# Kernel optimization log

Measured on AMD Instinct MI355X. Metric: run time of the kernel, lower is better.

The kernel has to match this reference:

```python
import jax, jax.numpy as jnp
import numpy as np

D_MODEL = 2048
K_DIM = 128
V_DIM = 128
H = 16
B = 1
S = 2048
SCALE_BASE = 512.0
THETA = 10000.0
EPS = 1e-5


def setup_inputs() -> dict:
    key = jax.random.key(0)
    ks = jax.random.split(key, 11)
    lin = lambda k, i, o: jax.random.normal(k, (i, o), jnp.float32) * 0.02
    return {
        "x": jax.random.normal(ks[0], (B, S, D_MODEL), jnp.float32),
        "Wq": lin(ks[1], D_MODEL, K_DIM * H), "bq": jnp.zeros((K_DIM * H,), jnp.float32),
        "Wk": lin(ks[2], D_MODEL, K_DIM * H), "bk": jnp.zeros((K_DIM * H,), jnp.float32),
        "Wv": lin(ks[3], D_MODEL, V_DIM * H), "bv": jnp.zeros((V_DIM * H,), jnp.float32),
        "Wg": lin(ks[4], D_MODEL, V_DIM * H), "bg": jnp.zeros((V_DIM * H,), jnp.float32),
        "Wo": lin(ks[5], V_DIM * H, D_MODEL), "bo": jnp.zeros((D_MODEL,), jnp.float32),
    }


def _rotate_half(x):
    # interleaved pairs: (x0, x1, x2, x3, ...) -> (-x1, x0, -x3, x2, ...)
    xr = x.reshape(*x.shape[:-1], -1, 2)
    x1, x2 = xr[..., 0], xr[..., 1]
    return jnp.stack((-x2, x1), axis=-1).reshape(x.shape)


def _rope_xpos(q, k, seq_len, dim):
    pos = jnp.arange(seq_len, dtype=jnp.float32)
    inv_freq = 1.0 / (THETA ** (jnp.arange(0, dim, 2, dtype=jnp.float32) / dim))
    freqs = jnp.repeat(pos[:, None] * inv_freq[None, :], 2, axis=-1)  # (S, dim)
    cos, sin = jnp.cos(freqs), jnp.sin(freqs)
    sbase = (jnp.arange(0, dim, 2, dtype=jnp.float32) + 0.4 * dim) / (1.4 * dim)
    power = (pos - seq_len // 2) / SCALE_BASE
    scale = jnp.repeat(sbase[None, :] ** power[:, None], 2, axis=-1)  # (S, dim)
    q = (q * cos + _rotate_half(q) * sin) * scale
    k = (k * cos + _rotate_half(k) * sin) / scale
    return q, k


def reference(x, Wq, bq, Wk, bk, Wv, bv, Wg, bg, Wo, bo):
    Bb, Ss, Dd = x.shape
    heads = lambda t: t.reshape(Bb, Ss, H, -1).transpose(0, 2, 1, 3)  # (B,H,S,d)
    q = heads(x @ Wq + bq)
    k = heads(x @ Wk + bk)
    v = heads(x @ Wv + bv)
    q, k = _rope_xpos(q, k, Ss, K_DIM)
    # per-head decay gamma_h = 1 - 2^{-5-h}
    gamma = 1.0 - 2.0 ** (-5.0 - jnp.arange(H, dtype=jnp.float32))
    pos = jnp.arange(Ss, dtype=jnp.float32)
    pm = pos[:, None] - pos[None, :]  # (S,S)
    decay_mask = jnp.where(pm >= 0, gamma[:, None, None] ** jnp.maximum(pm, 0.0), 0.0)  # (H,S,S)
    scores = jnp.einsum('bhid,bhjd->bhij', q, k) * decay_mask
    ret = jnp.einsum('bhij,bhjd->bhid', scores, v)  # (B,H,S,V_DIM)
    # concat heads and GroupNorm (num_groups=H, affine=False) over flattened rows
    concat = ret.transpose(0, 2, 1, 3).reshape(Bb * Ss, H, V_DIM)
    mu = concat.mean(-1, keepdims=True)
    var = ((concat - mu) ** 2).mean(-1, keepdims=True)
    gn = ((concat - mu) / jnp.sqrt(var + EPS)).reshape(Bb, Ss, H * V_DIM)
    out = (jax.nn.silu(x @ Wg + bg) * gn) @ Wo + bo
    return out
```

## Files before the change

### kernel.cpp

```cpp
#include <hip/hip_runtime.h>
#include <hip/hip_bf16.h>

#define S 2048
#define DM 2048
#define H 16
#define HD 128

using bf16 = __hip_bfloat16;
typedef __attribute__((ext_vector_type(8))) short bf16x8;
typedef __attribute__((ext_vector_type(8))) unsigned short u16x8;
typedef __attribute__((ext_vector_type(4))) float f32x4;

__device__ __forceinline__ unsigned short f2bu(float f) {
  bf16 b = __float2bfloat16(f);
  union { bf16 b; unsigned short u; } cv; cv.b = b; return cv.u;
}
__device__ __forceinline__ float bu2f(unsigned short u) {
  union { bf16 b; unsigned short u; } cv; cv.u = u; return __bfloat162float(cv.b);
}

__device__ __forceinline__ void async_copy16(const void* g, void* l) {
  __builtin_amdgcn_global_load_lds(
      (const __attribute__((address_space(1))) void*)g,
      (__attribute__((address_space(3))) void*)l, 16, 0, 0);
}

__global__ __launch_bounds__(256) void cvt_kernel(const float* __restrict__ x,
                                                  unsigned short* __restrict__ o) {
  int i = (blockIdx.x * 256 + threadIdx.x) * 4;
  float4 v = *(const float4*)(x + i);
  ushort4 r;
  r.x = f2bu(v.x); r.y = f2bu(v.y); r.z = f2bu(v.z); r.w = f2bu(v.w);
  *(ushort4*)(o + i) = r;
}

__global__ __launch_bounds__(256) void wtrans_kernel(
    const float* __restrict__ s0, const float* __restrict__ s1, const float* __restrict__ s2,
    const float* __restrict__ s3, const float* __restrict__ s4,
    unsigned short* __restrict__ d0, unsigned short* __restrict__ d1, unsigned short* __restrict__ d2,
    unsigned short* __restrict__ d3, unsigned short* __restrict__ d4) {
  __shared__ float tile[64][65];
  int z = blockIdx.z;
  const float* src = z == 0 ? s0 : z == 1 ? s1 : z == 2 ? s2 : z == 3 ? s3 : s4;
  unsigned short* dst = z == 0 ? d0 : z == 1 ? d1 : z == 2 ? d2 : z == 3 ? d3 : d4;
  int tid = threadIdx.x;
  int by = blockIdx.y * 64;
  int bx = blockIdx.x * 64;
  int r0 = tid >> 4;
  int c0 = (tid & 15) * 4;
#pragma unroll
  for (int i = 0; i < 4; i++) {
    int row = r0 + i * 16;
    float4 t = *(const float4*)(src + (size_t)(by + row) * DM + bx + c0);
    tile[row][c0 + 0] = t.x; tile[row][c0 + 1] = t.y;
    tile[row][c0 + 2] = t.z; tile[row][c0 + 3] = t.w;
  }
  __syncthreads();
#pragma unroll
  for (int i = 0; i < 4; i++) {
    int nrow = r0 + i * 16;
    ushort4 o;
    o.x = f2bu(tile[c0 + 0][nrow]);
    o.y = f2bu(tile[c0 + 1][nrow]);
    o.z = f2bu(tile[c0 + 2][nrow]);
    o.w = f2bu(tile[c0 + 3][nrow]);
    *(ushort4*)(dst + (size_t)(bx + nrow) * DM + by + c0) = o;
  }
}

__device__ __forceinline__ void stage_half(const unsigned short* gbase, char* ldsbase, int tid) {
#pragma unroll
  for (int r = 0; r < 2; r++) {
    int a = r * 8192 + tid * 16;
    int row = a >> 7;
    int cb = (a & 127) ^ ((row & 7) << 4);
    async_copy16((const unsigned char*)(gbase + (size_t)row * DM) + cb, ldsbase + a);
  }
}

__global__ __launch_bounds__(512, 2) void gemm_qkvg_kernel(
    const unsigned short* __restrict__ A, const unsigned short* __restrict__ Bm,
    const float* __restrict__ bias0, const float* __restrict__ bias1,
    const float* __restrict__ bias2, const float* __restrict__ bias3,
    unsigned short* __restrict__ C0, unsigned short* __restrict__ C1,
    unsigned short* __restrict__ Vt, unsigned short* __restrict__ C3) {
  __shared__ alignas(16) char smem[131072];
  char* sA = smem;
  char* sB = smem + 65536;
  int tid = threadIdx.x;
  int wg = blockIdx.y * 32 + blockIdx.x;
  int swz = (wg & 7) * 32 + (wg >> 3);
  int bm = (swz >> 5) * 256;
  int bn = (swz & 31) * 256;
  int wid = tid >> 6, lane = tid & 63;
  int wm = wid >> 2, wn = wid & 3;
  int r16 = lane & 15, quad = lane >> 4;
  f32x4 acc[8][4] = {};
  bf16x8 bfrag[2][4];
  const int bhalf = (wn >> 1) << 14;
  const int blr0 = ((wn & 1) << 6) + r16;

  stage_half(Bm + (size_t)bn * DM, sB, tid);
  stage_half(Bm + (size_t)(bn + 128) * DM, sB + 16384, tid);
  stage_half(A + (size_t)bm * DM, sA, tid);
  stage_half(A + (size_t)(bm + 128) * DM, sA + 16384, tid);
  asm volatile("s_waitcnt vmcnt(0)" ::: "memory");
  __builtin_amdgcn_s_barrier();

  for (int t = 0; t < 32; ++t) {
    const int buf = (t & 1) << 15;
    const int nbuf = buf ^ 32768;
    const bool more = t < 31;
    const int kn = (t + 1) * 64;
    char* sAc = sA + buf;
    char* sBc = sB + buf;
    bf16x8 afrag[4];

#pragma unroll
    for (int nt = 0; nt < 4; ++nt) {
      int lr = blr0 + nt * 16;
      bfrag[0][nt] = *(const bf16x8*)(sBc + bhalf + lr * 128 + ((quad * 16) ^ ((lr & 7) << 4)));
    }
#pragma unroll
    for (int mt = 0; mt < 4; ++mt) {
      int lr = mt * 32 + wm * 16 + r16;
      afrag[mt] = *(const bf16x8*)(sAc + lr * 128 + ((quad * 16) ^ ((lr & 7) << 4)));
    }
    if (more) {
      stage_half(Bm + (size_t)bn * DM + kn, sB + nbuf, tid);
      stage_half(Bm + (size_t)(bn + 128) * DM + kn, sB + nbuf + 16384, tid);
      stage_half(A + (size_t)bm * DM + kn, sA + nbuf, tid);
      stage_half(A + (size_t)(bm + 128) * DM + kn, sA + nbuf + 16384, tid);
    }
    __builtin_amdgcn_s_barrier();
    asm volatile("s_waitcnt lgkmcnt(0)" ::: "memory");
    __builtin_amdgcn_s_setprio(1);
#pragma unroll
    for (int mt = 0; mt < 4; ++mt)
#pragma unroll
      for (int nt = 0; nt < 4; ++nt)
        acc[mt][nt] = __builtin_amdgcn_mfma_f32_16x16x32_bf16(afrag[mt], bfrag[0][nt], acc[mt][nt], 0, 0, 0);
    __builtin_amdgcn_s_setprio(0);

#pragma unroll
    for (int nt = 0; nt < 4; ++nt) {
      int lr = blr0 + nt * 16;
      bfrag[1][nt] = *(const bf16x8*)(sBc + bhalf + lr * 128 + ((64 + quad * 16) ^ ((lr & 7) << 4)));
    }
#pragma unroll
    for (int mt = 0; mt < 4; ++mt) {
      int lr = mt * 32 + wm * 16 + r16;
      afrag[mt] = *(const bf16x8*)(sAc + lr * 128 + ((64 + quad * 16) ^ ((lr & 7) << 4)));
    }
    __builtin_amdgcn_s_barrier();
    asm volatile("s_waitcnt lgkmcnt(0)" ::: "memory");
    __builtin_amdgcn_s_setprio(1);
#pragma unroll
    for (int mt = 0; mt < 4; ++mt)
#pragma unroll
      for (int nt = 0; nt < 4; ++nt)
        acc[mt][nt] = __builtin_amdgcn_mfma_f32_16x16x32_bf16(afrag[mt], bfrag[1][nt], acc[mt][nt], 0, 0, 0);
    __builtin_amdgcn_s_setprio(0);

#pragma unroll
    for (int mt = 0; mt < 4; ++mt) {
      int lr = mt * 32 + wm * 16 + r16;
      afrag[mt] = *(const bf16x8*)(sAc + 16384 + lr * 128 + ((quad * 16) ^ ((lr & 7) << 4)));
    }
    __builtin_amdgcn_s_barrier();
    asm volatile("s_waitcnt lgkmcnt(0)" ::: "memory");
    __builtin_amdgcn_s_setprio(1);
#pragma unroll
    for (int mt = 0; mt < 4; ++mt)
#pragma unroll
      for (int nt = 0; nt < 4; ++nt)
        acc[4 + mt][nt] = __builtin_amdgcn_mfma_f32_16x16x32_bf16(afrag[mt], bfrag[0][nt], acc[4 + mt][nt], 0, 0, 0);
    __builtin_amdgcn_s_setprio(0);

#pragma unroll
    for (int mt = 0; mt < 4; ++mt) {
      int lr = mt * 32 + wm * 16 + r16;
      afrag[mt] = *(const bf16x8*)(sAc + 16384 + lr * 128 + ((64 + quad * 16) ^ ((lr & 7) << 4)));
    }
    __builtin_amdgcn_s_barrier();
    asm volatile("s_waitcnt lgkmcnt(0)" ::: "memory");
    __builtin_amdgcn_s_setprio(1);
#pragma unroll
    for (int mt = 0; mt < 4; ++mt)
#pragma unroll
      for (int nt = 0; nt < 4; ++nt)
        acc[4 + mt][nt] = __builtin_amdgcn_mfma_f32_16x16x32_bf16(afrag[mt], bfrag[1][nt], acc[4 + mt][nt], 0, 0, 0);
    __builtin_amdgcn_s_setprio(0);

    asm volatile("s_waitcnt vmcnt(0)" ::: "memory");
    __builtin_amdgcn_s_barrier();
  }

  int ch = bn >> 11;
  const float* bp = ch == 0 ? bias0 : ch == 1 ? bias1 : ch == 2 ? bias2 : bias3;
  int lcb = bn & 2047;
  if (ch == 2) {
#pragma unroll
    for (int nt = 0; nt < 4; ++nt) {
      int lc = lcb + wn * 64 + nt * 16 + r16;
      float bv = bp[lc];
#pragma unroll
      for (int mt = 0; mt < 8; ++mt) {
        int m0 = bm + (mt >> 2) * 128 + (mt & 3) * 32 + wm * 16 + quad * 4;
        ushort4 o;
        o.x = f2bu(acc[mt][nt][0] + bv);
        o.y = f2bu(acc[mt][nt][1] + bv);
        o.z = f2bu(acc[mt][nt][2] + bv);
        o.w = f2bu(acc[mt][nt][3] + bv);
        *(ushort4*)(Vt + (size_t)lc * DM + m0) = o;
      }
    }
  } else {
    unsigned short* Cp = ch == 0 ? C0 : ch == 1 ? C1 : C3;
#pragma unroll
    for (int nt = 0; nt < 4; ++nt) {
      int lc = lcb + wn * 64 + nt * 16 + r16;
      float bv = bp[lc];
#pragma unroll
      for (int mt = 0; mt < 8; ++mt) {
        int m0 = bm + (mt >> 2) * 128 + (mt & 3) * 32 + wm * 16 + quad * 4;
#pragma unroll
        for (int rr = 0; rr < 4; ++rr)
          Cp[(size_t)(m0 + rr) * DM + lc] = f2bu(acc[mt][nt][rr] + bv);
      }
    }
  }
}

__global__ __launch_bounds__(256) void gemm_out_kernel(
    const unsigned short* __restrict__ A, const unsigned short* __restrict__ Bp,
    const float* __restrict__ bias, float* __restrict__ C) {
  __shared__ alignas(16) unsigned char sA[16384];
  __shared__ alignas(16) unsigned char sB[16384];
  int tid = threadIdx.x;
  int bm = blockIdx.y * 128, bn = blockIdx.x * 128;
  int wid = tid >> 6, lane = tid & 63;
  int wm = wid >> 1, wn = wid & 1;
  int r16 = lane & 15, quad = lane >> 4;
  f32x4 acc[4][4] = {};
  for (int kt = 0; kt < DM; kt += 64) {
#pragma unroll
    for (int r = 0; r < 4; r++) {
      int a = r * 4096 + tid * 16;
      int row = a >> 7;
      int cb = (a & 127) ^ ((row & 7) << 4);
      async_copy16((const unsigned char*)(A + (size_t)(bm + row) * DM + kt) + cb, sA + a);
      async_copy16((const unsigned char*)(Bp + (size_t)(bn + row) * DM + kt) + cb, sB + a);
    }
    __syncthreads();
#pragma unroll
    for (int kk = 0; kk < 2; kk++) {
      bf16x8 af[4], bfr[4];
#pragma unroll
      for (int mt = 0; mt < 4; mt++) {
        int row = wm * 64 + mt * 16 + r16;
        af[mt] = *(const bf16x8*)(sA + row * 128 + ((quad * 16 + kk * 64) ^ ((row & 7) << 4)));
      }
#pragma unroll
      for (int nt = 0; nt < 4; nt++) {
        int row = wn * 64 + nt * 16 + r16;
        bfr[nt] = *(const bf16x8*)(sB + row * 128 + ((quad * 16 + kk * 64) ^ ((row & 7) << 4)));
      }
#pragma unroll
      for (int mt = 0; mt < 4; mt++)
#pragma unroll
        for (int nt = 0; nt < 4; nt++)
          acc[mt][nt] = __builtin_amdgcn_mfma_f32_16x16x32_bf16(af[mt], bfr[nt], acc[mt][nt], 0, 0, 0);
    }
    __syncthreads();
  }
#pragma unroll
  for (int nt = 0; nt < 4; nt++) {
    int n = bn + wn * 64 + nt * 16 + r16;
    float bv = bias[n];
#pragma unroll
    for (int mt = 0; mt < 4; mt++) {
      int m0 = bm + wm * 64 + mt * 16 + quad * 4;
#pragma unroll
      for (int r = 0; r < 4; r++)
        C[(size_t)(m0 + r) * DM + n] = acc[mt][nt][r] + bv;
    }
  }
}

__global__ __launch_bounds__(256) void rope_kernel(unsigned short* __restrict__ q,
                                                   unsigned short* __restrict__ k) {
  int idx = blockIdx.x * 256 + threadIdx.x;
  int s = idx >> 10;
  int p = idx & 1023;
  int t = p & 63;
  int head = p >> 6;
  int col = (head << 7) + (t << 1);
  size_t off = (size_t)s * DM + col;
  float ang = (float)s * exp2f((float)(-2 * t) * (13.287712379549449f / 128.0f));
  float sn, cs;
  sincosf(ang, &sn, &cs);
  float sb = ((float)(2 * t) + 51.2f) * (1.0f / 179.2f);
  float power = ((float)s - 1024.0f) * (1.0f / 512.0f);
  float scale = exp2f(power * log2f(sb));
  float l2g = log2f(1.0f - exp2f((float)(-5 - head)));
  float qsc = scale * exp2f((float)s * l2g);
  float ksc = (1.0f / scale) * exp2f(-(float)s * l2g);
  unsigned int qu = *(unsigned int*)(q + off);
  float a = bu2f(qu & 0xffff), b = bu2f(qu >> 16);
  float qa = (a * cs - b * sn) * qsc;
  float qb2 = (b * cs + a * sn) * qsc;
  *(unsigned int*)(q + off) = (unsigned int)f2bu(qa) | ((unsigned int)f2bu(qb2) << 16);
  unsigned int ku = *(unsigned int*)(k + off);
  float c2 = bu2f(ku & 0xffff), d2 = bu2f(ku >> 16);
  float ka = (c2 * cs - d2 * sn) * ksc;
  float kb2 = (d2 * cs + c2 * sn) * ksc;
  *(unsigned int*)(k + off) = (unsigned int)f2bu(ka) | ((unsigned int)f2bu(kb2) << 16);
}

__device__ __forceinline__ void stage_kv(const unsigned short* __restrict__ k,
                                         const unsigned short* __restrict__ vt,
                                         int h, int J0, unsigned char* dK,
                                         unsigned char* dV, int tid) {
#pragma unroll
  for (int r = 0; r < 4; r++) {
    int a = r * 4096 + tid * 16;
    int rowk = a >> 8;
    int cbk = (a & 255) ^ ((rowk & 7) << 4);
    async_copy16((const unsigned char*)(k + (size_t)(J0 + rowk) * DM + h * HD) + cbk, dK + a);
    int rowv = a >> 7;
    int cbv = (a & 127) ^ ((rowv & 7) << 4);
    async_copy16((const unsigned char*)(vt + (size_t)(h * HD + rowv) * DM + J0) + cbv, dV + a);
  }
}

__global__ __launch_bounds__(256) void retention_kernel(
    const unsigned short* __restrict__ q, const unsigned short* __restrict__ k,
    const unsigned short* __restrict__ vt, const unsigned short* __restrict__ g,
    unsigned short* __restrict__ y) {
  __shared__ alignas(16) unsigned char sK[2][16384];
  __shared__ alignas(16) unsigned char sV[2][16384];
  __shared__ alignas(16) unsigned char Plds[8192];
  int bx = blockIdx.x;
  int hi = bx >> 8;
  int h = ((bx >> 5) & 7) | (hi << 3);
  int ib = hi ? (bx & 31) : (31 - (bx & 31));
  int I = ib << 6;
  int tid = threadIdx.x, wid = tid >> 6, lane = tid & 63;
  int r16 = lane & 15, quad = lane >> 4;
  bf16x8 aQ[4];
  size_t qrow = (size_t)(I + wid * 16 + r16);
#pragma unroll
  for (int kk = 0; kk < 4; kk++)
    aQ[kk] = *(const bf16x8*)(q + qrow * DM + h * HD + kk * 32 + quad * 8);
  f32x4 acc[8] = {};
  unsigned char* Pw = Plds + wid * 2048;
  stage_kv(k, vt, h, 0, sK[0], sV[0], tid);
  for (int J0 = 0; J0 <= I; J0 += 64) {
    int cur = (J0 >> 6) & 1;
    bool more = (J0 + 64) <= I;
    if (more) stage_kv(k, vt, h, J0 + 64, sK[cur ^ 1], sV[cur ^ 1], tid);
    if (more) { asm volatile("s_waitcnt vmcnt(8)" ::: "memory"); }
    else      { asm volatile("s_waitcnt vmcnt(0)" ::: "memory"); }
    __builtin_amdgcn_s_barrier();
    const unsigned char* sKc = sK[cur];
    const unsigned char* sVc = sV[cur];
    f32x4 sf[4] = {};
#pragma unroll
    for (int nt = 0; nt < 4; nt++) {
      int row = nt * 16 + r16;
#pragma unroll
      for (int kk = 0; kk < 4; kk++) {
        bf16x8 bK = *(const bf16x8*)(sKc + row * 256 + ((kk * 64 + quad * 16) ^ ((row & 7) << 4)));
        sf[nt] = __builtin_amdgcn_mfma_f32_16x16x32_bf16(aQ[kk], bK, sf[nt], 0, 0, 0);
      }
    }
    bool diag = (J0 == I);
#pragma unroll
    for (int nt = 0; nt < 4; nt++) {
      int j = nt * 16 + r16;
#pragma unroll
      for (int r = 0; r < 4; r++) {
        int ii = wid * 16 + quad * 4 + r;
        float pv = sf[nt][r];
        if (diag && (ii - j) < 0) pv = 0.0f;
        int pr = quad * 4 + r;
        int pcb = (nt * 16 + r16) * 2;
        *(unsigned short*)(Pw + pr * 128 + (pcb ^ ((pr & 7) << 4))) = f2bu(pv);
      }
    }
#pragma unroll
    for (int kk2 = 0; kk2 < 2; kk2++) {
      int cb = kk2 * 64 + quad * 16;
      bf16x8 aP = *(const bf16x8*)(Pw + r16 * 128 + (cb ^ ((r16 & 7) << 4)));
#pragma unroll
      for (int nt2 = 0; nt2 < 8; nt2++) {
        int row = nt2 * 16 + r16;
        bf16x8 bV = *(const bf16x8*)(sVc + row * 128 + ((kk2 * 64 + quad * 16) ^ ((row & 7) << 4)));
        acc[nt2] = __builtin_amdgcn_mfma_f32_16x16x32_bf16(aP, bV, acc[nt2], 0, 0, 0);
      }
    }
    __builtin_amdgcn_s_barrier();
  }
#pragma unroll
  for (int r = 0; r < 4; r++) {
    float sum = 0.0f, sq = 0.0f;
#pragma unroll
    for (int nt2 = 0; nt2 < 8; nt2++) {
      float v = acc[nt2][r];
      sum += v; sq += v * v;
    }
#pragma unroll
    for (int o = 1; o <= 8; o <<= 1) {
      sum += __shfl_xor(sum, o, 64);
      sq += __shfl_xor(sq, o, 64);
    }
    float mean = sum * 0.0078125f;
    float var = sq * 0.0078125f - mean * mean;
    float rstd = rsqrtf(var + 1e-5f);
    int i = I + wid * 16 + quad * 4 + r;
    size_t rowbase = (size_t)i * DM + h * HD;
#pragma unroll
    for (int nt2 = 0; nt2 < 8; nt2++) {
      int col = nt2 * 16 + r16;
      float gv = bu2f(g[rowbase + col]);
      float sg = gv / (1.0f + expf(-gv));
      float yv = sg * (acc[nt2][r] - mean) * rstd;
      y[rowbase + col] = f2bu(yv);
    }
  }
}

extern "C" void kernel_launch(void* const* d_in, const int* in_sizes, int n_in,
                              void* d_out, int out_size, void* d_ws, size_t ws_size,
                              hipStream_t stream) {
  (void)in_sizes; (void)n_in; (void)out_size; (void)ws_size;
  const float* x  = (const float*)d_in[0];
  const float* Wq = (const float*)d_in[1];
  const float* bq = (const float*)d_in[2];
  const float* Wk = (const float*)d_in[3];
  const float* bk = (const float*)d_in[4];
  const float* Wv = (const float*)d_in[5];
  const float* bv = (const float*)d_in[6];
  const float* Wg = (const float*)d_in[7];
  const float* bg = (const float*)d_in[8];
  const float* Wo = (const float*)d_in[9];
  const float* bo = (const float*)d_in[10];

  char* ws = (char*)d_ws;
  const size_t MB = 1ull << 20;
  unsigned short* xb   = (unsigned short*)(ws + 0 * MB);
  unsigned short* wcat = (unsigned short*)(ws + 8 * MB);
  unsigned short* wto  = (unsigned short*)(ws + 40 * MB);
  unsigned short* qb   = (unsigned short*)(ws + 48 * MB);
  unsigned short* kb   = (unsigned short*)(ws + 56 * MB);
  unsigned short* gb   = (unsigned short*)(ws + 72 * MB);
  unsigned short* vt   = (unsigned short*)(ws + 80 * MB);
  unsigned short* yb   = (unsigned short*)(ws + 104 * MB);

  cvt_kernel<<<4096, 256, 0, stream>>>(x, xb);
  wtrans_kernel<<<dim3(32, 32, 5), 256, 0, stream>>>(
      Wq, Wk, Wv, Wg, Wo,
      wcat, wcat + (size_t)2048 * DM, wcat + (size_t)4096 * DM, wcat + (size_t)6144 * DM, wto);
  gemm_qkvg_kernel<<<dim3(32, 8), 512, 0, stream>>>(
      xb, wcat, bq, bk, bv, bg, qb, kb, vt, gb);
  rope_kernel<<<8192, 256, 0, stream>>>(qb, kb);
  retention_kernel<<<512, 256, 0, stream>>>(qb, kb, vt, gb, yb);
  gemm_out_kernel<<<dim3(16, 16), 256, 0, stream>>>(yb, wto, bo, (float*)d_out);
}
```

Baseline: 184.9 us.

## Double-buffer output GEMM with narrower tiles; load V directly to registers in retention

The output projection GEMM now uses 128x64 tiles, which doubles the grid to 512 blocks. It double-buffers LDS with async prefetch of the next K slice and remaps block indices in a swizzled order for cache locality. In the retention kernel, V tiles are no longer staged in LDS. Each wave now loads its V fragments straight from global memory into registers, which halves LDS use and may raise occupancy. The cost is more global traffic and register pressure, and a full vmcnt(0) wait at each iteration end that could expose latency.

```diff
diff --git a/kernel.cpp b/kernel.cpp
--- a/kernel.cpp
+++ b/kernel.cpp
@@ -232,51 +232,74 @@
   }
 }
 
+__device__ __forceinline__ void stage_o(const unsigned short* gA, const unsigned short* gB,
+                                        char* dA, char* dB, int tid) {
+#pragma unroll
+  for (int r = 0; r < 4; r++) {
+    int a = r * 4096 + tid * 16;
+    int row = a >> 7;
+    int cb = (a & 127) ^ ((row & 7) << 4);
+    async_copy16((const unsigned char*)(gA + (size_t)row * DM) + cb, dA + a);
+  }
+#pragma unroll
+  for (int r = 0; r < 2; r++) {
+    int a = r * 4096 + tid * 16;
+    int row = a >> 7;
+    int cb = (a & 127) ^ ((row & 7) << 4);
+    async_copy16((const unsigned char*)(gB + (size_t)row * DM) + cb, dB + a);
+  }
+}
+
 __global__ __launch_bounds__(256) void gemm_out_kernel(
     const unsigned short* __restrict__ A, const unsigned short* __restrict__ Bp,
     const float* __restrict__ bias, float* __restrict__ C) {
-  __shared__ alignas(16) unsigned char sA[16384];
-  __shared__ alignas(16) unsigned char sB[16384];
+  __shared__ alignas(16) char sA[2][16384];
+  __shared__ alignas(16) char sB[2][8192];
   int tid = threadIdx.x;
-  int bm = blockIdx.y * 128, bn = blockIdx.x * 128;
+  int wg = blockIdx.y * 32 + blockIdx.x;
+  int swz = (wg & 7) * 64 + (wg >> 3);
+  int bm = (swz >> 5) * 128;
+  int bn = (swz & 31) * 64;
   int wid = tid >> 6, lane = tid & 63;
   int wm = wid >> 1, wn = wid & 1;
   int r16 = lane & 15, quad = lane >> 4;
-  f32x4 acc[4][4] = {};
-  for (int kt = 0; kt < DM; kt += 64) {
-#pragma unroll
-    for (int r = 0; r < 4; r++) {
-      int a = r * 4096 + tid * 16;
-      int row = a >> 7;
-      int cb = (a & 127) ^ ((row & 7) << 4);
-      async_copy16((const unsigned char*)(A + (size_t)(bm + row) * DM + kt) + cb, sA + a);
-      async_copy16((const unsigned char*)(Bp + (size_t)(bn + row) * DM + kt) + cb, sB + a);
-    }
-    __syncthreads();
+  f32x4 acc[4][2] = {};
+
+  stage_o(A + (size_t)bm * DM, Bp + (size_t)bn * DM, sA[0], sB[0], tid);
+  asm volatile("s_waitcnt vmcnt(0)" ::: "memory");
+  __builtin_amdgcn_s_barrier();
+
+  for (int t = 0; t < 32; ++t) {
+    int cur = t & 1;
+    bool more = t < 31;
+    int kn = (t + 1) * 64;
+    if (more)
+      stage_o(A + (size_t)bm * DM + kn, Bp + (size_t)bn * DM + kn, sA[cur ^ 1], sB[cur ^ 1], tid);
 #pragma unroll
     for (int kk = 0; kk < 2; kk++) {
-      bf16x8 af[4], bfr[4];
+      bf16x8 af[4], bfr[2];
 #pragma unroll
       for (int mt = 0; mt < 4; mt++) {
         int row = wm * 64 + mt * 16 + r16;
-        af[mt] = *(const bf16x8*)(sA + row * 128 + ((quad * 16 + kk * 64) ^ ((row & 7) << 4)));
-      }
-#pragma unroll
-      for (int nt = 0; nt < 4; nt++) {
-        int row = wn * 64 + nt * 16 + r16;
-        bfr[nt] = *(const bf16x8*)(sB + row * 128 + ((quad * 16 + kk * 64) ^ ((row & 7) << 4)));
+        af[mt] = *(const bf16x8*)(sA[cur] + row * 128 + ((kk * 64 + quad * 16) ^ ((row & 7) << 4)));
+      }
+#pragma unroll
+      for (int nt = 0; nt < 2; nt++) {
+        int row = wn * 32 + nt * 16 + r16;
+        bfr[nt] = *(const bf16x8*)(sB[cur] + row * 128 + ((kk * 64 + quad * 16) ^ ((row & 7) << 4)));
       }
 #pragma unroll
       for (int mt = 0; mt < 4; mt++)
 #pragma unroll
-        for (int nt = 0; nt < 4; nt++)
+        for (int nt = 0; nt < 2; nt++)
           acc[mt][nt] = __builtin_amdgcn_mfma_f32_16x16x32_bf16(af[mt], bfr[nt], acc[mt][nt], 0, 0, 0);
     }
-    __syncthreads();
-  }
-#pragma unroll
-  for (int nt = 0; nt < 4; nt++) {
-    int n = bn + wn * 64 + nt * 16 + r16;
+    asm volatile("s_waitcnt vmcnt(0)" ::: "memory");
+    __builtin_amdgcn_s_barrier();
+  }
+#pragma unroll
+  for (int nt = 0; nt < 2; nt++) {
+    int n = bn + wn * 32 + nt * 16 + r16;
     float bv = bias[n];
 #pragma unroll
     for (int mt = 0; mt < 4; mt++) {
@@ -318,19 +341,14 @@
   *(unsigned int*)(k + off) = (unsigned int)f2bu(ka) | ((unsigned int)f2bu(kb2) << 16);
 }
 
-__device__ __forceinline__ void stage_kv(const unsigned short* __restrict__ k,
-                                         const unsigned short* __restrict__ vt,
-                                         int h, int J0, unsigned char* dK,
-                                         unsigned char* dV, int tid) {
+__device__ __forceinline__ void stage_k(const unsigned short* __restrict__ k,
+                                        int h, int J0, unsigned char* dK, int tid) {
 #pragma unroll
   for (int r = 0; r < 4; r++) {
     int a = r * 4096 + tid * 16;
     int rowk = a >> 8;
     int cbk = (a & 255) ^ ((rowk & 7) << 4);
     async_copy16((const unsigned char*)(k + (size_t)(J0 + rowk) * DM + h * HD) + cbk, dK + a);
-    int rowv = a >> 7;
-    int cbv = (a & 127) ^ ((rowv & 7) << 4);
-    async_copy16((const unsigned char*)(vt + (size_t)(h * HD + rowv) * DM + J0) + cbv, dV + a);
   }
 }
 
@@ -339,7 +357,6 @@
     const unsigned short* __restrict__ vt, const unsigned short* __restrict__ g,
     unsigned short* __restrict__ y) {
   __shared__ alignas(16) unsigned char sK[2][16384];
-  __shared__ alignas(16) unsigned char sV[2][16384];
   __shared__ alignas(16) unsigned char Plds[8192];
   int bx = blockIdx.x;
   int hi = bx >> 8;
@@ -355,16 +372,20 @@
     aQ[kk] = *(const bf16x8*)(q + qrow * DM + h * HD + kk * 32 + quad * 8);
   f32x4 acc[8] = {};
   unsigned char* Pw = Plds + wid * 2048;
-  stage_kv(k, vt, h, 0, sK[0], sV[0], tid);
+  stage_k(k, h, 0, sK[0], tid);
+  asm volatile("s_waitcnt vmcnt(0)" ::: "memory");
+  __builtin_amdgcn_s_barrier();
   for (int J0 = 0; J0 <= I; J0 += 64) {
     int cur = (J0 >> 6) & 1;
     bool more = (J0 + 64) <= I;
-    if (more) stage_kv(k, vt, h, J0 + 64, sK[cur ^ 1], sV[cur ^ 1], tid);
-    if (more) { asm volatile("s_waitcnt vmcnt(8)" ::: "memory"); }
-    else      { asm volatile("s_waitcnt vmcnt(0)" ::: "memory"); }
-    __builtin_amdgcn_s_barrier();
+    bf16x8 bV[2][8];
+#pragma unroll
+    for (int kk2 = 0; kk2 < 2; kk2++)
+#pragma unroll
+      for (int nt2 = 0; nt2 < 8; nt2++)
+        bV[kk2][nt2] = *(const bf16x8*)(vt + (size_t)(h * HD + nt2 * 16 + r16) * DM + J0 + kk2 * 32 + quad * 8);
+    if (more) stage_k(k, h, J0 + 64, sK[cur ^ 1], tid);
     const unsigned char* sKc = sK[cur];
-    const unsigned char* sVc = sV[cur];
     f32x4 sf[4] = {};
 #pragma unroll
     for (int nt = 0; nt < 4; nt++) {
@@ -394,12 +415,10 @@
       int cb = kk2 * 64 + quad * 16;
       bf16x8 aP = *(const bf16x8*)(Pw + r16 * 128 + (cb ^ ((r16 & 7) << 4)));
 #pragma unroll
-      for (int nt2 = 0; nt2 < 8; nt2++) {
-        int row = nt2 * 16 + r16;
-        bf16x8 bV = *(const bf16x8*)(sVc + row * 128 + ((kk2 * 64 + quad * 16) ^ ((row & 7) << 4)));
-        acc[nt2] = __builtin_amdgcn_mfma_f32_16x16x32_bf16(aP, bV, acc[nt2], 0, 0, 0);
-      }
-    }
+      for (int nt2 = 0; nt2 < 8; nt2++)
+        acc[nt2] = __builtin_amdgcn_mfma_f32_16x16x32_bf16(aP, bV[kk2][nt2], acc[nt2], 0, 0, 0);
+    }
+    asm volatile("s_waitcnt vmcnt(0)" ::: "memory");
     __builtin_amdgcn_s_barrier();
   }
 #pragma unroll
@@ -466,5 +485,5 @@
       xb, wcat, bq, bk, bv, bg, qb, kb, vt, gb);
   rope_kernel<<<8192, 256, 0, stream>>>(qb, kb);
   retention_kernel<<<512, 256, 0, stream>>>(qb, kb, vt, gb, yb);
-  gemm_out_kernel<<<dim3(16, 16), 256, 0, stream>>>(yb, wto, bo, (float*)d_out);
-}
+  gemm_out_kernel<<<dim3(32, 16), 256, 0, stream>>>(yb, wto, bo, (float*)d_out);
+}
```

Result: slower. 224.7 us (+21.6%).
